# Performance work log

Measured on AMD Instinct MI355X. Metric: run time of the kernel, lower is better.

## Reference

```python
import jax, jax.numpy as jnp
import numpy as np

B, T, D, H = 4, 2048, 1024, 16
HD = D // H


def setup_inputs() -> dict:
    key = jax.random.key(0)
    ks = jax.random.split(key, 9)
    s = 1.0 / np.sqrt(D)
    return {
        "x": jax.random.normal(ks[0], (B, T, D), dtype=jnp.float32),
        "Wq": jax.random.normal(ks[1], (D, D), dtype=jnp.float32) * s,
        "bq": jnp.zeros((D,), dtype=jnp.float32),
        "Wk": jax.random.normal(ks[2], (D, D), dtype=jnp.float32) * s,
        "bk": jnp.zeros((D,), dtype=jnp.float32),
        "Wv": jax.random.normal(ks[3], (D, D), dtype=jnp.float32) * s,
        "bv": jnp.zeros((D,), dtype=jnp.float32),
        "Wo": jax.random.normal(ks[4], (D, D), dtype=jnp.float32) * s,
        "bo": jnp.zeros((D,), dtype=jnp.float32),
    }


def reference(x, Wq, bq, Wk, bk, Wv, bv, Wo, bo):
    b, t, c = x.shape
    h, hd = H, HD
    scale = hd ** -0.5
    # projections: [B,T,C] -> [B,H,T,hd]
    q = (x @ Wq.T + bq).reshape(b, t, h, hd).transpose(0, 2, 1, 3)
    k = (x @ Wk.T + bk).reshape(b, t, h, hd).transpose(0, 2, 1, 3)
    v = (x @ Wv.T + bv).reshape(b, t, h, hd).transpose(0, 2, 1, 3)
    # scores [B,H,T,T], causal mask (no kv cache path, T > 1)
    attn = jnp.einsum("bhqd,bhkd->bhqk", q, k) * scale
    causal = jnp.triu(jnp.ones((t, t), dtype=bool), k=1)
    attn = jnp.where(causal, -jnp.inf, attn)
    attn = jax.nn.softmax(attn, axis=-1)
    out = jnp.einsum("bhqk,bhkd->bhqd", attn, v)
    out = out.transpose(0, 2, 1, 3).reshape(b, t, c)
    return (out @ Wo.T + bo, k, v)
```

## Files before the change

### kernel.cpp

```cpp
#include <hip/hip_runtime.h>
#include <hip/hip_bf16.h>
#include <cstdint>


typedef short bf16x8 __attribute__((ext_vector_type(8)));
typedef float f32x4 __attribute__((ext_vector_type(4)));

#define GLDS16(g, l)                                                          \
  __builtin_amdgcn_global_load_lds(                                           \
      (const __attribute__((address_space(1))) void*)(g),                     \
      (__attribute__((address_space(3))) void*)(l), 16, 0, 0)

static __device__ __forceinline__ short f2b(float f) {
  union { float f; unsigned u; } x; x.f = f;
  unsigned r = (x.u + 0x7FFFu + ((x.u >> 16) & 1u)) >> 16;
  return (short)r;
}

static __device__ __forceinline__ unsigned pack2bf(float a, float b) {
  union { __hip_bfloat162 h; unsigned u; } c;
  c.h = __float22bfloat162_rn(make_float2(a, b));
  return c.u;
}

__global__ void cvt_f32_bf16(const float* __restrict__ src, short* __restrict__ dst, int n4) {
  int i = blockIdx.x * blockDim.x + threadIdx.x;
  if (i < n4) {
    float4 v = ((const float4*)src)[i];
    short4 o; o.x = f2b(v.x); o.y = f2b(v.y); o.z = f2b(v.z); o.w = f2b(v.w);
    ((short4*)dst)[i] = o;
  }
}

template <int MODE>
__global__ __launch_bounds__(256) void gemm_bt(
    const short* __restrict__ A, const short* __restrict__ Bm,
    const float* __restrict__ bias,
    float* __restrict__ out_f, short* __restrict__ out_b) {
  __shared__ short As[128 * 32];
  __shared__ short Bs[128 * 32];
  const int t = threadIdx.x;
  const int lane = t & 63;
  const int w = t >> 6;
  const int wm = w >> 1, wn = w & 1;
  const int quad = lane >> 4, l15 = lane & 15;
  const int bm = blockIdx.y, bn = blockIdx.x;

  f32x4 acc[4][4];
  for (int i = 0; i < 4; i++)
    for (int j = 0; j < 4; j++) acc[i][j] = (f32x4){0.f, 0.f, 0.f, 0.f};

  const int c0 = t, c1 = t + 256;
  const int r0 = c0 >> 2, cc0 = c0 & 3;
  const int r1 = c1 >> 2, cc1 = c1 & 3;
  const short* Abase = A + (size_t)bm * 128 * 1024;
  const short* Bbase = Bm + (size_t)bn * 128 * 1024;

  for (int kk = 0; kk < 1024; kk += 32) {
    __syncthreads();
    GLDS16(Abase + (size_t)r0 * 1024 + kk + cc0 * 8, &As[c0 * 8]);
    GLDS16(Abase + (size_t)r1 * 1024 + kk + cc1 * 8, &As[c1 * 8]);
    GLDS16(Bbase + (size_t)r0 * 1024 + kk + cc0 * 8, &Bs[c0 * 8]);
    GLDS16(Bbase + (size_t)r1 * 1024 + kk + cc1 * 8, &Bs[c1 * 8]);
    __syncthreads();
    bf16x8 af[4], bfr[4];
    for (int mt = 0; mt < 4; mt++)
      af[mt] = *(const bf16x8*)(As + (wm * 64 + mt * 16 + l15) * 32 + quad * 8);
    for (int nt = 0; nt < 4; nt++)
      bfr[nt] = *(const bf16x8*)(Bs + (wn * 64 + nt * 16 + l15) * 32 + quad * 8);
    for (int mt = 0; mt < 4; mt++)
      for (int nt = 0; nt < 4; nt++)
        acc[mt][nt] = __builtin_amdgcn_mfma_f32_16x16x32_bf16(af[mt], bfr[nt], acc[mt][nt], 0, 0, 0);
  }

  for (int mt = 0; mt < 4; mt++) {
    const int row_base = bm * 128 + wm * 64 + mt * 16 + quad * 4;
    for (int nt = 0; nt < 4; nt++) {
      const int col = bn * 128 + wn * 64 + nt * 16 + l15;
      const float bb = bias[col];
      for (int r = 0; r < 4; r++) {
        const int row = row_base + r;
        const float v = acc[mt][nt][r] + bb;
        if (MODE == 3) {
          out_f[(size_t)row * 1024 + col] = v;
        } else {
          const int b = row >> 11, tt = row & 2047;
          const int h = col >> 6, hi = col & 63;
          const size_t idx = (((size_t)(b * 16 + h)) * 2048 + tt) * 64 + hi;
          if (MODE == 0) {
            out_b[idx] = f2b(v);
          } else if (MODE == 1) {
            out_f[idx] = v; out_b[idx] = f2b(v);
          } else {
            out_f[idx] = v;
            out_b[(((size_t)(b * 16 + h)) * 64 + hi) * 2048 + tt] = f2b(v);
          }
        }
      }
    }
  }
}

__global__ __launch_bounds__(256) void attn_fwd(
    const short* __restrict__ Qb, const short* __restrict__ Kb,
    const short* __restrict__ VTb, short* __restrict__ Ob) {
  __shared__ short Ks[128 * 64];
  __shared__ short VTs[64 * 128];
  __shared__ short Plds[4][16 * 136];
  const int t = threadIdx.x;
  const int w = t >> 6;
  const int lane = t & 63;
  const int quad = lane >> 4, l15 = lane & 15;
  const int bh = blockIdx.y;
  const int b = bh >> 4, h = bh & 15;
  const int qt = (blockIdx.x + blockIdx.y) & 31;
  const int q0 = qt * 64 + w * 16;

  const short* Qh = Qb + (size_t)bh * 2048 * 64;
  const short* Kh = Kb + (size_t)bh * 2048 * 64;
  const short* VTh = VTb + (size_t)bh * 64 * 2048;
  short* Pw = &Plds[w][0];

  const bf16x8 qf0 = *(const bf16x8*)(Qh + (q0 + l15) * 64 + quad * 8);
  const bf16x8 qf1 = *(const bf16x8*)(Qh + (q0 + l15) * 64 + quad * 8 + 32);

  float m_q = -1e30f, l_q = 0.f;
  f32x4 o[4];
  for (int nt = 0; nt < 4; nt++) o[nt] = (f32x4){0.f, 0.f, 0.f, 0.f};

  const int ntile = (qt >> 1) + 1;
  const float sscale = 0.125f * 1.4426950408889634f;

  for (int jt = 0; jt < ntile; ++jt) {
    const int j0 = jt << 7;
    __syncthreads();
    for (int rr = 0; rr < 4; rr++) {
      const int c = rr * 256 + t;
      const int row = c >> 3, colL = c & 7;
      const int colg = colL ^ (row & 7);
      GLDS16(Kh + (size_t)(j0 + row) * 64 + colg * 8, &Ks[c * 8]);
    }
    for (int rr = 0; rr < 4; rr++) {
      const int c = rr * 256 + t;
      const int row = c >> 4, colL = c & 15;
      const int colg = colL ^ (row & 7);
      GLDS16(VTh + (size_t)row * 2048 + j0 + colg * 8, &VTs[c * 8]);
    }
    __syncthreads();

    float sv[8][4];
    for (int si = 0; si < 8; ++si) {
      const int r = si * 16 + l15;
      bf16x8 kf0 = *(const bf16x8*)&Ks[(r * 8 + (quad ^ (r & 7))) * 8];
      bf16x8 kf1 = *(const bf16x8*)&Ks[(r * 8 + ((quad ^ 4) ^ (r & 7))) * 8];
      f32x4 z = (f32x4){0.f, 0.f, 0.f, 0.f};
      z = __builtin_amdgcn_mfma_f32_16x16x32_bf16(kf0, qf0, z, 0, 0, 0);
      z = __builtin_amdgcn_mfma_f32_16x16x32_bf16(kf1, qf1, z, 0, 0, 0);
      for (int r4 = 0; r4 < 4; r4++) sv[si][r4] = z[r4] * sscale;
    }
    if (jt == ntile - 1) {
      const int qg = q0 + l15;
      for (int si = 0; si < 8; si++) {
        const int kbase = j0 + si * 16 + quad * 4;
        for (int r4 = 0; r4 < 4; r4++)
          if (kbase + r4 > qg) sv[si][r4] = -1e30f;
      }
    }
    float vmax = sv[0][0];
    for (int si = 0; si < 8; si++)
      for (int r4 = 0; r4 < 4; r4++) vmax = fmaxf(vmax, sv[si][r4]);
    vmax = fmaxf(vmax, __shfl_xor(vmax, 16));
    vmax = fmaxf(vmax, __shfl_xor(vmax, 32));
    const float mn = fmaxf(m_q, vmax);
    const float alpha = exp2f(m_q - mn);
    m_q = mn;
    float ssum = 0.f;
    for (int si = 0; si < 8; si++) {
      float p0 = exp2f(sv[si][0] - mn);
      float p1 = exp2f(sv[si][1] - mn);
      float p2 = exp2f(sv[si][2] - mn);
      float p3 = exp2f(sv[si][3] - mn);
      ssum += (p0 + p1) + (p2 + p3);
      uint2 pk; pk.x = pack2bf(p0, p1); pk.y = pack2bf(p2, p3);
      *(uint2*)(Pw + l15 * 136 + si * 16 + quad * 4) = pk;
    }
    ssum += __shfl_xor(ssum, 16);
    ssum += __shfl_xor(ssum, 32);
    l_q = l_q * alpha + ssum;
    float ar[4];
    for (int r4 = 0; r4 < 4; r4++) ar[r4] = __shfl(alpha, quad * 4 + r4);
    for (int nt = 0; nt < 4; nt++)
      for (int r4 = 0; r4 < 4; r4++) o[nt][r4] *= ar[r4];
    for (int kc = 0; kc < 4; kc++) {
      bf16x8 pf = *(const bf16x8*)(Pw + l15 * 136 + kc * 32 + quad * 8);
      for (int nt = 0; nt < 4; nt++) {
        const int rv = nt * 16 + l15;
        bf16x8 vf = *(const bf16x8*)&VTs[(rv * 16 + ((kc * 4 + quad) ^ (rv & 7))) * 8];
        o[nt] = __builtin_amdgcn_mfma_f32_16x16x32_bf16(pf, vf, o[nt], 0, 0, 0);
      }
    }
  }
  float lr[4];
  for (int r4 = 0; r4 < 4; r4++) lr[r4] = __shfl(l_q, quad * 4 + r4);
  for (int nt = 0; nt < 4; nt++) {
    const int col = h * 64 + nt * 16 + l15;
    for (int r4 = 0; r4 < 4; r4++) {
      const int q = q0 + quad * 4 + r4;
      Ob[((size_t)b * 2048 + q) * 1024 + col] = f2b(o[nt][r4] / lr[r4]);
    }
  }
}

extern "C" void kernel_launch(void* const* d_in, const int* in_sizes, int n_in,
                              void* d_out, int out_size, void* d_ws, size_t ws_size,
                              hipStream_t stream) {
  const float* x  = (const float*)d_in[0];
  const float* Wq = (const float*)d_in[1];
  const float* bq = (const float*)d_in[2];
  const float* Wk = (const float*)d_in[3];
  const float* bk = (const float*)d_in[4];
  const float* Wv = (const float*)d_in[5];
  const float* bv = (const float*)d_in[6];
  const float* Wo = (const float*)d_in[7];
  const float* bo = (const float*)d_in[8];

  float* out   = (float*)d_out;
  float* k_out = out + (size_t)8388608;
  float* v_out = out + (size_t)16777216;

  short* ws  = (short*)d_ws;
  short* xb   = ws;
  short* wqb  = ws + 8388608;
  short* wkb  = ws + 9437184;
  short* wvb  = ws + 10485760;
  short* wob  = ws + 11534336;
  short* qb   = ws + 12582912;
  short* kb   = ws + 20971520;
  short* vtb  = ws + 29360128;
  short* attb = ws + 37748736;

  cvt_f32_bf16<<<8192, 256, 0, stream>>>(x,  xb,  2097152);
  cvt_f32_bf16<<<1024, 256, 0, stream>>>(Wq, wqb, 262144);
  cvt_f32_bf16<<<1024, 256, 0, stream>>>(Wk, wkb, 262144);
  cvt_f32_bf16<<<1024, 256, 0, stream>>>(Wv, wvb, 262144);
  cvt_f32_bf16<<<1024, 256, 0, stream>>>(Wo, wob, 262144);

  dim3 g(8, 64), blk(256);
  gemm_bt<0><<<g, blk, 0, stream>>>(xb, wqb, bq, nullptr, qb);
  gemm_bt<1><<<g, blk, 0, stream>>>(xb, wkb, bk, k_out, kb);
  gemm_bt<2><<<g, blk, 0, stream>>>(xb, wvb, bv, v_out, vtb);

  attn_fwd<<<dim3(32, 64), 256, 0, stream>>>(qb, kb, vtb, attb);

  gemm_bt<3><<<g, blk, 0, stream>>>(attb, wob, bo, out, nullptr);
}
```

Baseline: 398.9 us.

## Fuse QKV GEMMs and weight casts, pair causal tiles in attention

The four weight conversions become one launch, and the three QKV projection GEMMs become a single launch whose grid selects the weight. The attention kernel now has each block process two mirrored query tiles (qt and 31-qt), evening out causal work, and reorders blocks across heads. It reuses the K LDS buffer for P with an XOR swizzle, skips the O rescale when no row max changes, folds the scale into an fma before exp2, and uses hardware exp2, rcp and packed bf16 convert instructions. This cuts launch overhead, causal load imbalance and ALU work, at the cost of an extra barrier per tile and slightly lower-precision math intrinsics.

Result: faster. 356.3 us (-10.7%).

```diff
diff --git a/kernel.cpp b/kernel.cpp
--- a/kernel.cpp
+++ b/kernel.cpp
@@ -17,10 +17,10 @@
   return (short)r;
 }
 
-static __device__ __forceinline__ unsigned pack2bf(float a, float b) {
-  union { __hip_bfloat162 h; unsigned u; } c;
-  c.h = __float22bfloat162_rn(make_float2(a, b));
-  return c.u;
+static __device__ __forceinline__ unsigned cvtpk2(float a, float b) {
+  unsigned r;
+  asm("v_cvt_pk_bf16_f32 %0, %1, %2" : "=v"(r) : "v"(a), "v"(b));
+  return r;
 }
 
 __global__ void cvt_f32_bf16(const float* __restrict__ src, short* __restrict__ dst, int n4) {
@@ -30,6 +30,17 @@
     short4 o; o.x = f2b(v.x); o.y = f2b(v.y); o.z = f2b(v.z); o.w = f2b(v.w);
     ((short4*)dst)[i] = o;
   }
+}
+
+__global__ void cvt_w4(const float* __restrict__ a, const float* __restrict__ b,
+                       const float* __restrict__ c, const float* __restrict__ d,
+                       short* __restrict__ dst) {
+  int i = blockIdx.x * blockDim.x + threadIdx.x;
+  int sel = i >> 18, j = i & 262143;
+  const float* src = sel == 0 ? a : sel == 1 ? b : sel == 2 ? c : d;
+  float4 v = ((const float4*)src)[j];
+  short4 o; o.x = f2b(v.x); o.y = f2b(v.y); o.z = f2b(v.z); o.w = f2b(v.w);
+  ((short4*)dst)[i] = o;
 }
 
 template <int MODE>
@@ -101,112 +112,197 @@
   }
 }
 
-__global__ __launch_bounds__(256) void attn_fwd(
+__global__ __launch_bounds__(256) void gemm_qkv(
+    const short* __restrict__ A,
+    const short* __restrict__ W0, const short* __restrict__ W1, const short* __restrict__ W2,
+    const float* __restrict__ b0, const float* __restrict__ b1, const float* __restrict__ b2,
+    float* __restrict__ kf, float* __restrict__ vf,
+    short* __restrict__ qbo, short* __restrict__ kbo, short* __restrict__ vtbo) {
+  __shared__ short As[128 * 32];
+  __shared__ short Bs[128 * 32];
+  const int t = threadIdx.x;
+  const int lane = t & 63;
+  const int w = t >> 6;
+  const int wm = w >> 1, wn = w & 1;
+  const int quad = lane >> 4, l15 = lane & 15;
+  const int bm = blockIdx.y;
+  const int sel = blockIdx.x >> 3, bn = blockIdx.x & 7;
+  const short* Bm = sel == 0 ? W0 : (sel == 1 ? W1 : W2);
+  const float* bias = sel == 0 ? b0 : (sel == 1 ? b1 : b2);
+
+  f32x4 acc[4][4];
+  for (int i = 0; i < 4; i++)
+    for (int j = 0; j < 4; j++) acc[i][j] = (f32x4){0.f, 0.f, 0.f, 0.f};
+
+  const int c0 = t, c1 = t + 256;
+  const int r0 = c0 >> 2, cc0 = c0 & 3;
+  const int r1 = c1 >> 2, cc1 = c1 & 3;
+  const short* Abase = A + (size_t)bm * 128 * 1024;
+  const short* Bbase = Bm + (size_t)bn * 128 * 1024;
+
+  for (int kk = 0; kk < 1024; kk += 32) {
+    __syncthreads();
+    GLDS16(Abase + (size_t)r0 * 1024 + kk + cc0 * 8, &As[c0 * 8]);
+    GLDS16(Abase + (size_t)r1 * 1024 + kk + cc1 * 8, &As[c1 * 8]);
+    GLDS16(Bbase + (size_t)r0 * 1024 + kk + cc0 * 8, &Bs[c0 * 8]);
+    GLDS16(Bbase + (size_t)r1 * 1024 + kk + cc1 * 8, &Bs[c1 * 8]);
+    __syncthreads();
+    bf16x8 af[4], bfr[4];
+    for (int mt = 0; mt < 4; mt++)
+      af[mt] = *(const bf16x8*)(As + (wm * 64 + mt * 16 + l15) * 32 + quad * 8);
+    for (int nt = 0; nt < 4; nt++)
+      bfr[nt] = *(const bf16x8*)(Bs + (wn * 64 + nt * 16 + l15) * 32 + quad * 8);
+    for (int mt = 0; mt < 4; mt++)
+      for (int nt = 0; nt < 4; nt++)
+        acc[mt][nt] = __builtin_amdgcn_mfma_f32_16x16x32_bf16(af[mt], bfr[nt], acc[mt][nt], 0, 0, 0);
+  }
+
+  for (int mt = 0; mt < 4; mt++) {
+    const int row_base = bm * 128 + wm * 64 + mt * 16 + quad * 4;
+    for (int nt = 0; nt < 4; nt++) {
+      const int col = bn * 128 + wn * 64 + nt * 16 + l15;
+      const float bb = bias[col];
+      for (int r = 0; r < 4; r++) {
+        const int row = row_base + r;
+        const float v = acc[mt][nt][r] + bb;
+        const int b = row >> 11, tt = row & 2047;
+        const int h = col >> 6, hi = col & 63;
+        const size_t idx = (((size_t)(b * 16 + h)) * 2048 + tt) * 64 + hi;
+        if (sel == 0) {
+          qbo[idx] = f2b(v);
+        } else if (sel == 1) {
+          kf[idx] = v; kbo[idx] = f2b(v);
+        } else {
+          vf[idx] = v;
+          vtbo[(((size_t)(b * 16 + h)) * 64 + hi) * 2048 + tt] = f2b(v);
+        }
+      }
+    }
+  }
+}
+
+__global__ __launch_bounds__(256, 4) void attn_fwd(
     const short* __restrict__ Qb, const short* __restrict__ Kb,
     const short* __restrict__ VTb, short* __restrict__ Ob) {
   __shared__ short Ks[128 * 64];
   __shared__ short VTs[64 * 128];
-  __shared__ short Plds[4][16 * 136];
   const int t = threadIdx.x;
   const int w = t >> 6;
   const int lane = t & 63;
   const int quad = lane >> 4, l15 = lane & 15;
-  const int bh = blockIdx.y;
+
+  const int L = blockIdx.x + (blockIdx.y << 4);
+  const int work = ((L & 7) << 7) + (L >> 3);
+  const int bh = work >> 4;
+  const int base = work & 15;
   const int b = bh >> 4, h = bh & 15;
-  const int qt = (blockIdx.x + blockIdx.y) & 31;
-  const int q0 = qt * 64 + w * 16;
 
   const short* Qh = Qb + (size_t)bh * 2048 * 64;
   const short* Kh = Kb + (size_t)bh * 2048 * 64;
   const short* VTh = VTb + (size_t)bh * 64 * 2048;
-  short* Pw = &Plds[w][0];
-
-  const bf16x8 qf0 = *(const bf16x8*)(Qh + (q0 + l15) * 64 + quad * 8);
-  const bf16x8 qf1 = *(const bf16x8*)(Qh + (q0 + l15) * 64 + quad * 8 + 32);
-
-  float m_q = -1e30f, l_q = 0.f;
-  f32x4 o[4];
-  for (int nt = 0; nt < 4; nt++) o[nt] = (f32x4){0.f, 0.f, 0.f, 0.f};
-
-  const int ntile = (qt >> 1) + 1;
+  unsigned* Pd = (unsigned*)Ks + w * 1024;
+  const int swz = (l15 & 7) << 2;
   const float sscale = 0.125f * 1.4426950408889634f;
 
-  for (int jt = 0; jt < ntile; ++jt) {
-    const int j0 = jt << 7;
-    __syncthreads();
-    for (int rr = 0; rr < 4; rr++) {
-      const int c = rr * 256 + t;
-      const int row = c >> 3, colL = c & 7;
-      const int colg = colL ^ (row & 7);
-      GLDS16(Kh + (size_t)(j0 + row) * 64 + colg * 8, &Ks[c * 8]);
+  for (int s = 0; s < 2; ++s) {
+    const int qt = s ? (31 - base) : base;
+    const int q0 = qt * 64 + w * 16;
+    const bf16x8 qf0 = *(const bf16x8*)(Qh + (q0 + l15) * 64 + quad * 8);
+    const bf16x8 qf1 = *(const bf16x8*)(Qh + (q0 + l15) * 64 + quad * 8 + 32);
+
+    float m_q = -1e30f, l_q = 0.f;
+    f32x4 o[4];
+    for (int nt = 0; nt < 4; nt++) o[nt] = (f32x4){0.f, 0.f, 0.f, 0.f};
+    const int ntile = (qt >> 1) + 1;
+
+    for (int jt = 0; jt < ntile; ++jt) {
+      const int j0 = jt << 7;
+      __syncthreads();
+      for (int rr = 0; rr < 4; rr++) {
+        const int c = rr * 256 + t;
+        const int row = c >> 3, colL = c & 7;
+        const int colg = colL ^ (row & 7);
+        GLDS16(Kh + (size_t)(j0 + row) * 64 + colg * 8, &Ks[c * 8]);
+      }
+      for (int rr = 0; rr < 4; rr++) {
+        const int c = rr * 256 + t;
+        const int row = c >> 4, colL = c & 15;
+        const int colg = colL ^ (row & 7);
+        GLDS16(VTh + (size_t)row * 2048 + j0 + colg * 8, &VTs[c * 8]);
+      }
+      __syncthreads();
+
+      float sv[8][4];
+      for (int si = 0; si < 8; ++si) {
+        const int r = si * 16 + l15;
+        bf16x8 kf0 = *(const bf16x8*)&Ks[(r * 8 + (quad ^ (r & 7))) * 8];
+        bf16x8 kf1 = *(const bf16x8*)&Ks[(r * 8 + ((quad ^ 4) ^ (r & 7))) * 8];
+        f32x4 z = (f32x4){0.f, 0.f, 0.f, 0.f};
+        z = __builtin_amdgcn_mfma_f32_16x16x32_bf16(kf0, qf0, z, 0, 0, 0);
+        z = __builtin_amdgcn_mfma_f32_16x16x32_bf16(kf1, qf1, z, 0, 0, 0);
+        for (int r4 = 0; r4 < 4; r4++) sv[si][r4] = z[r4];
+      }
+      if (jt == ntile - 1) {
+        const int qg = q0 + l15;
+        for (int si = 0; si < 8; si++) {
+          const int kbase = j0 + si * 16 + quad * 4;
+          for (int r4 = 0; r4 < 4; r4++)
+            if (kbase + r4 > qg) sv[si][r4] = -1e30f;
+        }
+      }
+      float vmax = fmaxf(fmaxf(sv[0][0], sv[0][1]), fmaxf(sv[0][2], sv[0][3]));
+      for (int si = 1; si < 8; si++) {
+        float m2 = fmaxf(fmaxf(sv[si][0], sv[si][1]), fmaxf(sv[si][2], sv[si][3]));
+        vmax = fmaxf(vmax, m2);
+      }
+      vmax = fmaxf(vmax, __shfl_xor(vmax, 16));
+      vmax = fmaxf(vmax, __shfl_xor(vmax, 32));
+      const float mn = fmaxf(m_q, vmax);
+      if (__any(vmax > m_q)) {
+        const float alpha = __builtin_amdgcn_exp2f((m_q - mn) * sscale);
+        l_q *= alpha;
+        float ar[4];
+        for (int r4 = 0; r4 < 4; r4++) ar[r4] = __shfl(alpha, quad * 4 + r4);
+        for (int nt = 0; nt < 4; nt++)
+          for (int r4 = 0; r4 < 4; r4++) o[nt][r4] *= ar[r4];
+      }
+      m_q = mn;
+      __syncthreads();
+
+      const float negmns = -mn * sscale;
+      float ssum = 0.f;
+      for (int si = 0; si < 8; si++) {
+        float p0 = __builtin_amdgcn_exp2f(fmaf(sv[si][0], sscale, negmns));
+        float p1 = __builtin_amdgcn_exp2f(fmaf(sv[si][1], sscale, negmns));
+        float p2 = __builtin_amdgcn_exp2f(fmaf(sv[si][2], sscale, negmns));
+        float p3 = __builtin_amdgcn_exp2f(fmaf(sv[si][3], sscale, negmns));
+        ssum += (p0 + p1) + (p2 + p3);
+        uint2 pk; pk.x = cvtpk2(p0, p1); pk.y = cvtpk2(p2, p3);
+        *(uint2*)(Pd + l15 * 64 + ((si * 8 + quad * 2) ^ swz)) = pk;
+      }
+      ssum += __shfl_xor(ssum, 16);
+      ssum += __shfl_xor(ssum, 32);
+      l_q += ssum;
+
+      for (int kc = 0; kc < 4; kc++) {
+        bf16x8 pf = *(const bf16x8*)(Pd + l15 * 64 + ((kc * 16 + quad * 4) ^ swz));
+        for (int nt = 0; nt < 4; nt++) {
+          const int rv = nt * 16 + l15;
+          bf16x8 vf = *(const bf16x8*)&VTs[(rv * 16 + ((kc * 4 + quad) ^ (rv & 7))) * 8];
+          o[nt] = __builtin_amdgcn_mfma_f32_16x16x32_bf16(pf, vf, o[nt], 0, 0, 0);
+        }
+      }
     }
-    for (int rr = 0; rr < 4; rr++) {
-      const int c = rr * 256 + t;
-      const int row = c >> 4, colL = c & 15;
-      const int colg = colL ^ (row & 7);
-      GLDS16(VTh + (size_t)row * 2048 + j0 + colg * 8, &VTs[c * 8]);
-    }
-    __syncthreads();
-
-    float sv[8][4];
-    for (int si = 0; si < 8; ++si) {
-      const int r = si * 16 + l15;
-      bf16x8 kf0 = *(const bf16x8*)&Ks[(r * 8 + (quad ^ (r & 7))) * 8];
-      bf16x8 kf1 = *(const bf16x8*)&Ks[(r * 8 + ((quad ^ 4) ^ (r & 7))) * 8];
-      f32x4 z = (f32x4){0.f, 0.f, 0.f, 0.f};
-      z = __builtin_amdgcn_mfma_f32_16x16x32_bf16(kf0, qf0, z, 0, 0, 0);
-      z = __builtin_amdgcn_mfma_f32_16x16x32_bf16(kf1, qf1, z, 0, 0, 0);
-      for (int r4 = 0; r4 < 4; r4++) sv[si][r4] = z[r4] * sscale;
-    }
-    if (jt == ntile - 1) {
-      const int qg = q0 + l15;
-      for (int si = 0; si < 8; si++) {
-        const int kbase = j0 + si * 16 + quad * 4;
-        for (int r4 = 0; r4 < 4; r4++)
-          if (kbase + r4 > qg) sv[si][r4] = -1e30f;
-      }
-    }
-    float vmax = sv[0][0];
-    for (int si = 0; si < 8; si++)
-      for (int r4 = 0; r4 < 4; r4++) vmax = fmaxf(vmax, sv[si][r4]);
-    vmax = fmaxf(vmax, __shfl_xor(vmax, 16));
-    vmax = fmaxf(vmax, __shfl_xor(vmax, 32));
-    const float mn = fmaxf(m_q, vmax);
-    const float alpha = exp2f(m_q - mn);
-    m_q = mn;
-    float ssum = 0.f;
-    for (int si = 0; si < 8; si++) {
-      float p0 = exp2f(sv[si][0] - mn);
-      float p1 = exp2f(sv[si][1] - mn);
-      float p2 = exp2f(sv[si][2] - mn);
-      float p3 = exp2f(sv[si][3] - mn);
-      ssum += (p0 + p1) + (p2 + p3);
-      uint2 pk; pk.x = pack2bf(p0, p1); pk.y = pack2bf(p2, p3);
-      *(uint2*)(Pw + l15 * 136 + si * 16 + quad * 4) = pk;
-    }
-    ssum += __shfl_xor(ssum, 16);
-    ssum += __shfl_xor(ssum, 32);
-    l_q = l_q * alpha + ssum;
-    float ar[4];
-    for (int r4 = 0; r4 < 4; r4++) ar[r4] = __shfl(alpha, quad * 4 + r4);
-    for (int nt = 0; nt < 4; nt++)
-      for (int r4 = 0; r4 < 4; r4++) o[nt][r4] *= ar[r4];
-    for (int kc = 0; kc < 4; kc++) {
-      bf16x8 pf = *(const bf16x8*)(Pw + l15 * 136 + kc * 32 + quad * 8);
-      for (int nt = 0; nt < 4; nt++) {
-        const int rv = nt * 16 + l15;
-        bf16x8 vf = *(const bf16x8*)&VTs[(rv * 16 + ((kc * 4 + quad) ^ (rv & 7))) * 8];
-        o[nt] = __builtin_amdgcn_mfma_f32_16x16x32_bf16(pf, vf, o[nt], 0, 0, 0);
-      }
-    }
-  }
-  float lr[4];
-  for (int r4 = 0; r4 < 4; r4++) lr[r4] = __shfl(l_q, quad * 4 + r4);
-  for (int nt = 0; nt < 4; nt++) {
-    const int col = h * 64 + nt * 16 + l15;
-    for (int r4 = 0; r4 < 4; r4++) {
-      const int q = q0 + quad * 4 + r4;
-      Ob[((size_t)b * 2048 + q) * 1024 + col] = f2b(o[nt][r4] / lr[r4]);
+
+    float lr[4], ri[4];
+    for (int r4 = 0; r4 < 4; r4++) lr[r4] = __shfl(l_q, quad * 4 + r4);
+    for (int r4 = 0; r4 < 4; r4++) ri[r4] = __builtin_amdgcn_rcpf(lr[r4]);
+    for (int nt = 0; nt < 4; nt++) {
+      const int col = h * 64 + nt * 16 + l15;
+      for (int r4 = 0; r4 < 4; r4++) {
+        const int q = q0 + quad * 4 + r4;
+        Ob[((size_t)b * 2048 + q) * 1024 + col] = f2b(o[nt][r4] * ri[r4]);
+      }
     }
   }
 }
@@ -239,18 +335,13 @@
   short* vtb  = ws + 29360128;
   short* attb = ws + 37748736;
 
-  cvt_f32_bf16<<<8192, 256, 0, stream>>>(x,  xb,  2097152);
-  cvt_f32_bf16<<<1024, 256, 0, stream>>>(Wq, wqb, 262144);
-  cvt_f32_bf16<<<1024, 256, 0, stream>>>(Wk, wkb, 262144);
-  cvt_f32_bf16<<<1024, 256, 0, stream>>>(Wv, wvb, 262144);
-  cvt_f32_bf16<<<1024, 256, 0, stream>>>(Wo, wob, 262144);
-
-  dim3 g(8, 64), blk(256);
-  gemm_bt<0><<<g, blk, 0, stream>>>(xb, wqb, bq, nullptr, qb);
-  gemm_bt<1><<<g, blk, 0, stream>>>(xb, wkb, bk, k_out, kb);
-  gemm_bt<2><<<g, blk, 0, stream>>>(xb, wvb, bv, v_out, vtb);
-
-  attn_fwd<<<dim3(32, 64), 256, 0, stream>>>(qb, kb, vtb, attb);
-
-  gemm_bt<3><<<g, blk, 0, stream>>>(attb, wob, bo, out, nullptr);
-}
+  cvt_f32_bf16<<<8192, 256, 0, stream>>>(x, xb, 2097152);
+  cvt_w4<<<4096, 256, 0, stream>>>(Wq, Wk, Wv, Wo, wqb);
+
+  gemm_qkv<<<dim3(24, 64), 256, 0, stream>>>(
+      xb, wqb, wkb, wvb, bq, bk, bv, k_out, v_out, qb, kb, vtb);
+
+  attn_fwd<<<dim3(16, 64), 256, 0, stream>>>(qb, kb, vtb, attb);
+
+  gemm_bt<3><<<dim3(8, 64), 256, 0, stream>>>(attb, wob, bo, out, nullptr);
+}
```
